# Optimization experiments

Measured on AMD Instinct MI355X. Metric: run time of the kernel, lower is better.

Reference implementation:

```python
import jax, jax.numpy as jnp
import numpy as np

NUM_HEADS = 8
HEAD_DIM = 128
ATTN_SCALE = 0.12


def _rotary_tables(T, head_dim, dtype=jnp.float32):
    # modded-nanogpt half-truncated RoPE: rotate only first half of freq slots
    quarter = head_dim // 4
    angular = (1.0 / 1024.0) ** jnp.linspace(0.0, 1.0, quarter, dtype=dtype)
    angular = jnp.concatenate([angular, jnp.zeros(quarter, dtype=dtype)])  # [head_dim//2]
    t = jnp.arange(T, dtype=dtype)
    theta = t[:, None] * angular[None, :]  # [T, head_dim//2]
    return jnp.cos(theta), jnp.sin(theta)


def _apply_rotary(x, cos, sin):
    # x: [B, T, H, D]; cos/sin: [T, D//2]
    x1, x2 = jnp.split(x, 2, axis=-1)
    c = cos[None, :, None, :]
    s = sin[None, :, None, :]
    y1 = x1 * c + x2 * s
    y2 = -x1 * s + x2 * c
    return jnp.concatenate([y1, y2], axis=-1)


def _rms_norm(x):
    eps = jnp.asarray(jnp.finfo(x.dtype).eps, x.dtype)
    var = jnp.mean(jnp.square(x), axis=-1, keepdims=True)
    return x * jax.lax.rsqrt(var + eps)


def setup_inputs() -> dict:
    key = jax.random.key(0)
    k1, k2, k3, k4, k5 = jax.random.split(key, 5)
    B, T, D = 1, 4096, 1024
    hdim = NUM_HEADS * HEAD_DIM
    std = 0.5 * D ** (-0.5)
    x = jax.random.normal(k1, (B, T, D), dtype=jnp.float32)
    ve = jax.random.normal(k2, (B, T, hdim), dtype=jnp.float32)
    qkv_w = jax.random.normal(k3, (3, hdim, D), dtype=jnp.float32) * std
    lambdas = jnp.array([0.5, 0.5], dtype=jnp.float32)
    c_proj_w = jax.random.normal(k5, (D, hdim), dtype=jnp.float32) * std
    return {"x": x, "ve": ve, "qkv_w": qkv_w, "lambdas": lambdas, "c_proj_w": c_proj_w}


def reference(x, ve, qkv_w, lambdas, c_proj_w):
    B, T, D = x.shape
    H, Hd = NUM_HEADS, HEAD_DIM
    # QKV projection: qkv_w [3, H*Hd, D]
    qkv = jnp.einsum('btd,ckd->btck', x, qkv_w)  # [B, T, 3, H*Hd]
    qkv = qkv.reshape(B, T, 3, H, Hd)
    q, k, v = qkv[:, :, 0], qkv[:, :, 1], qkv[:, :, 2]  # [B, T, H, Hd]
    # QK RMSNorm
    q = _rms_norm(q)
    k = _rms_norm(k)
    # RoPE
    cos, sin = _rotary_tables(T, Hd, dtype=x.dtype)
    q = _apply_rotary(q, cos, sin)
    k = _apply_rotary(k, cos, sin)
    # value-embedding lambda mix
    v = lambdas[0] * v + lambdas[1] * ve.reshape(B, T, H, Hd)
    # causal attention with fixed scale 0.12 (block-causal FlexAttention mask)
    scores = jnp.einsum('bthd,bshd->bhts', q, k) * ATTN_SCALE  # [B, H, T, T]
    causal = jnp.tril(jnp.ones((T, T), dtype=bool))
    scores = jnp.where(causal[None, None], scores, jnp.asarray(-jnp.inf, scores.dtype))
    probs = jax.nn.softmax(scores, axis=-1)
    y = jnp.einsum('bhts,bshd->bthd', probs, v)  # [B, T, H, Hd]
    y = y.reshape(B, T, H * Hd)
    return y @ c_proj_w.T  # [B, T, D]
```

## Files before the change

kernel.cpp:

```cpp
#include <hip/hip_runtime.h>

typedef __bf16 bf16;
typedef __bf16 bf16x8 __attribute__((ext_vector_type(8)));
typedef __bf16 bf16x4 __attribute__((ext_vector_type(4)));
typedef __bf16 bf16x2 __attribute__((ext_vector_type(2)));
typedef float f32x4 __attribute__((ext_vector_type(4)));
typedef float f32x16 __attribute__((ext_vector_type(16)));
typedef int i32x4 __attribute__((ext_vector_type(4)));

#define GLL16(gp, lp)                                                          \
  __builtin_amdgcn_global_load_lds(                                            \
      (const __attribute__((address_space(1))) unsigned int*)(gp),             \
      (__attribute__((address_space(3))) unsigned int*)(lp), 16, 0, 0)

__global__ __launch_bounds__(256) void cast3_f32_bf16(
    const float* __restrict__ a, bf16* __restrict__ oa, int na4,
    const float* __restrict__ b, bf16* __restrict__ ob, int nb4,
    const float* __restrict__ c, bf16* __restrict__ oc, int nc4) {
  int i = blockIdx.x * blockDim.x + threadIdx.x;
  int stride = gridDim.x * blockDim.x;
  int total = na4 + nb4 + nc4;
  for (; i < total; i += stride) {
    const float4* src;
    bf16x4* dst;
    int j = i;
    if (j < na4) {
      src = (const float4*)a + j; dst = (bf16x4*)oa + j;
    } else if ((j -= na4) < nb4) {
      src = (const float4*)b + j; dst = (bf16x4*)ob + j;
    } else {
      j -= nb4;
      src = (const float4*)c + j; dst = (bf16x4*)oc + j;
    }
    float4 v = *src;
    bf16x4 o;
    o[0] = (bf16)v.x; o[1] = (bf16)v.y; o[2] = (bf16)v.z; o[3] = (bf16)v.w;
    *dst = o;
  }
}

template <int K, int LDC, typename CT>
__global__ __launch_bounds__(256) void gemm_bt(
    const bf16* __restrict__ A, const bf16* __restrict__ B,
    CT* __restrict__ C) {
  __shared__ __align__(16) bf16 As[128 * 64];
  __shared__ __align__(16) bf16 Bs[128 * 64];
  const int tid  = threadIdx.x;
  const int lane = tid & 63;
  const int wave = tid >> 6;
  const int ln15 = lane & 15, quad = lane >> 4;
  const int wm = wave >> 1, wn = wave & 1;
  const int m0 = blockIdx.y * 128, n0 = blockIdx.x * 128;

  f32x4 acc[4][4] = {};

  for (int k0 = 0; k0 < K; k0 += 64) {
    __syncthreads();
#pragma unroll
    for (int j = 0; j < 4; ++j) {
      int gbase = j * 256 + wave * 64;
      int g = gbase + lane;
      int r = g >> 3, c = (g & 7) ^ (r & 7);
      GLL16(A + (size_t)(m0 + r) * K + k0 + c * 8, As + (size_t)gbase * 8);
    }
#pragma unroll
    for (int j = 0; j < 4; ++j) {
      int gbase = j * 256 + wave * 64;
      int g = gbase + lane;
      int r = g >> 3, c = (g & 7) ^ (r & 7);
      GLL16(B + (size_t)(n0 + r) * K + k0 + c * 8, Bs + (size_t)gbase * 8);
    }
    __syncthreads();
#pragma unroll
    for (int kk = 0; kk < 2; ++kk) {
      bf16x8 af[4], bfr[4];
#pragma unroll
      for (int mi = 0; mi < 4; ++mi) {
        int m = wm * 64 + mi * 16 + ln15;
        int cg = kk * 4 + quad;
        af[mi] = *(const bf16x8*)(As + (m * 8 + (cg ^ (m & 7))) * 8);
      }
#pragma unroll
      for (int ni = 0; ni < 4; ++ni) {
        int n = wn * 64 + ni * 16 + ln15;
        int cg = kk * 4 + quad;
        bfr[ni] = *(const bf16x8*)(Bs + (n * 8 + (cg ^ (n & 7))) * 8);
      }
#pragma unroll
      for (int mi = 0; mi < 4; ++mi)
#pragma unroll
        for (int ni = 0; ni < 4; ++ni)
          acc[mi][ni] = __builtin_amdgcn_mfma_f32_16x16x32_bf16(
              af[mi], bfr[ni], acc[mi][ni], 0, 0, 0);
    }
  }
#pragma unroll
  for (int mi = 0; mi < 4; ++mi)
#pragma unroll
    for (int ni = 0; ni < 4; ++ni)
#pragma unroll
      for (int r = 0; r < 4; ++r) {
        int row = m0 + wm * 64 + mi * 16 + quad * 4 + r;
        int col = n0 + wn * 64 + ni * 16 + ln15;
        C[(size_t)row * LDC + col] = (CT)acc[mi][ni][r];
      }
}

__global__ __launch_bounds__(256) void qkv_post(
    const bf16* __restrict__ qkv, const float* __restrict__ ve,
    const float* __restrict__ lambdas, bf16* __restrict__ qn,
    bf16* __restrict__ kn, bf16* __restrict__ vt) {
  const int h  = blockIdx.x;
  const int t0 = blockIdx.y * 64;
  const int tid = threadIdx.x;
  const int wave = tid >> 6, lane = tid & 63;
  __shared__ __align__(16) float tile[64][129];

  const int j = lane;
  float cth = 1.0f, sth = 0.0f;
  for (int i = 0; i < 16; ++i) {
    int t = t0 + wave * 16 + i;
    if (j < 32) {
      float ang = exp2f((float)j * (-10.0f / 31.0f));
      float th = (float)t * ang;
      __sincosf(th, &sth, &cth);
    }
#pragma unroll
    for (int qk = 0; qk < 2; ++qk) {
      const bf16* row = qkv + (size_t)t * 3072 + qk * 1024 + h * 128;
      float x1 = (float)row[j], x2 = (float)row[j + 64];
      float ss = x1 * x1 + x2 * x2;
#pragma unroll
      for (int m = 1; m < 64; m <<= 1) ss += __shfl_xor(ss, m, 64);
      float rinv = rsqrtf(ss * (1.0f / 128.0f) + 1.1920929e-7f);
      if (qk == 0) rinv *= 0.12f;
      float y1 = (x1 * cth + x2 * sth) * rinv;
      float y2 = (x2 * cth - x1 * sth) * rinv;
      bf16* orow = (qk == 0 ? qn : kn) + (size_t)t * 1024 + h * 128;
      orow[j] = (bf16)y1;
      orow[j + 64] = (bf16)y2;
    }
  }

  float l0 = lambdas[0], l1 = lambdas[1];
  for (int c = 0; c < 32; ++c) {
    int idx = c * 256 + tid;
    int d = idx & 127, tl = idx >> 7;
    int t = t0 + tl;
    float v = (float)qkv[(size_t)t * 3072 + 2048 + h * 128 + d];
    float vev = ve[(size_t)t * 1024 + h * 128 + d];
    tile[tl][d] = l0 * v + l1 * vev;
  }
  __syncthreads();
  for (int c = 0; c < 32; ++c) {
    int idx = c * 256 + tid;
    int tl = idx & 63, d = idx >> 6;
    vt[((size_t)(h * 128 + d)) * 4096 + t0 + tl] = (bf16)tile[tl][d];
  }
}

__global__ __launch_bounds__(256, 2) void flash_attn(
    const bf16* __restrict__ qn, const bf16* __restrict__ kn,
    const bf16* __restrict__ vt, float* __restrict__ Op,
    float* __restrict__ ls) {
  const int id = blockIdx.x;
  const int qtile = 63 - (id >> 4);
  const int sub = id & 15;
  const int h = sub >> 1;
  const int half = sub & 1;
  const int tid = threadIdx.x;
  const int wave = tid >> 6, lane = tid & 63;
  const int l31 = lane & 31, hl = lane >> 5;
  const int qi = wave >> 1, ki = wave & 1;

  __shared__ __align__(16) bf16 smem[4 * 64 * 128];
  __shared__ float rsb[2][2][32];
  bf16* Ks = smem;
  bf16* Vs = smem + 2 * 64 * 128;

  const int q0 = qtile * 64;
  const int nkv = qtile + 1;
  const int half0 = (nkv + 1) >> 1;
  const int kt_begin = half ? half0 : 0;
  const int kt_end = half ? nkv : half0;
  const int niter = kt_end - kt_begin;
  const int pidx = (h * 64 + qtile) * 2 + half;

  if (niter == 0) {
    float4 z = {0.f, 0.f, 0.f, 0.f};
    float* opb = Op + (size_t)pidx * 8192;
#pragma unroll
    for (int j = 0; j < 8; ++j) *(float4*)(opb + tid * 32 + j * 4) = z;
    if (tid < 64) ls[pidx * 64 + tid] = 0.f;
    return;
  }

  const int qg = q0 + qi * 32 + l31;

  bf16x8 qf[8];
  {
    const bf16* qb = qn + (size_t)qg * 1024 + h * 128 + hl * 8;
#pragma unroll
    for (int f = 0; f < 8; ++f) qf[f] = *(const bf16x8*)(qb + f * 16);
  }

  f32x16 acc_o[4] = {};
  float rs = 0.0f;

  auto prefetch = [&](int kt, int buf) {
    const int kv0 = kt * 64;
    bf16* ks = Ks + buf * (64 * 128);
    bf16* vs = Vs + buf * (128 * 64);
#pragma unroll
    for (int jj = 0; jj < 4; ++jj) {
      int gbase = jj * 256 + wave * 64;
      int g = gbase + lane;
      int r = g >> 4, c = (g & 15) ^ (r & 15);
      GLL16(kn + (size_t)(kv0 + r) * 1024 + h * 128 + c * 8,
            ks + (size_t)gbase * 8);
    }
#pragma unroll
    for (int jj = 0; jj < 4; ++jj) {
      int gbase = jj * 256 + wave * 64;
      int g = gbase + lane;
      int d = g >> 3, c = (g & 7) ^ (d & 7);
      GLL16(vt + ((size_t)(h * 128 + d)) * 4096 + kv0 + c * 8,
            vs + (size_t)gbase * 8);
    }
  };

  prefetch(kt_begin, 0);

  for (int it = 0; it < niter; ++it) {
    const int kt = kt_begin + it;
    const int kv0 = kt * 64;
    __syncthreads();
    if (it + 1 < niter) prefetch(kt + 1, (it + 1) & 1);
    const bf16* ksb = Ks + (it & 1) * (64 * 128);
    const bf16* vsb = Vs + (it & 1) * (128 * 64);

    f32x16 accs = {};
    const int krow = ki * 32 + l31;
#pragma unroll
    for (int f = 0; f < 8; ++f) {
      bf16x8 a =
          *(const bf16x8*)(ksb + (krow * 16 + ((2 * f + hl) ^ (krow & 15))) * 8);
      accs = __builtin_amdgcn_mfma_f32_32x32x16_bf16(a, qf[f], accs, 0, 0, 0);
    }

    const bool diag = (kt == nkv - 1);
    float pe[16];
#pragma unroll
    for (int r = 0; r < 16; ++r) {
      int kvl = (r & 3) + 8 * (r >> 2) + 4 * hl;
      float v = __expf(accs[r]);
      if (diag && (kv0 + ki * 32 + kvl) > qg) v = 0.0f;
      rs += v;
      pe[r] = v;
    }
    int pk[8];
#pragma unroll
    for (int g = 0; g < 8; ++g) {
      bf16x2 t;
      t[0] = (bf16)pe[2 * g];
      t[1] = (bf16)pe[2 * g + 1];
      pk[g] = __builtin_bit_cast(int, t);
    }

    bf16x8 pf[2];
#pragma unroll
    for (int c = 0; c < 2; ++c) {
      int sh0 = __shfl_xor(pk[4 * c + 0], 32, 64);
      int sh1 = __shfl_xor(pk[4 * c + 1], 32, 64);
      int sh2 = __shfl_xor(pk[4 * c + 2], 32, 64);
      int sh3 = __shfl_xor(pk[4 * c + 3], 32, 64);
      int own0 = hl ? pk[4 * c + 2] : pk[4 * c + 0];
      int own1 = hl ? pk[4 * c + 3] : pk[4 * c + 1];
      int par0 = hl ? sh2 : sh0;
      int par1 = hl ? sh3 : sh1;
      i32x4 dv;
      dv[0] = hl ? par0 : own0;
      dv[1] = hl ? par1 : own1;
      dv[2] = hl ? own0 : par0;
      dv[3] = hl ? own1 : par1;
      pf[c] = __builtin_bit_cast(bf16x8, dv);
    }

#pragma unroll
    for (int dt = 0; dt < 4; ++dt) {
      int vrow = dt * 32 + l31;
#pragma unroll
      for (int c = 0; c < 2; ++c) {
        bf16x8 a = *(const bf16x8*)(
            vsb + (vrow * 8 + ((4 * ki + 2 * c + hl) ^ (vrow & 7))) * 8);
        acc_o[dt] =
            __builtin_amdgcn_mfma_f32_32x32x16_bf16(a, pf[c], acc_o[dt], 0, 0, 0);
      }
    }
  }

  rs += __shfl_xor(rs, 32, 64);
  __syncthreads();
  if (lane < 32) rsb[qi][ki][l31] = rs;
  float* ob = (float*)smem;
  if (ki == 1) {
#pragma unroll
    for (int dt = 0; dt < 4; ++dt)
#pragma unroll
      for (int r = 0; r < 16; ++r) {
        int d = dt * 32 + (r & 3) + 8 * (r >> 2) + 4 * hl;
        ob[(qi * 32 + l31) * 129 + d] = acc_o[dt][r];
      }
  }
  __syncthreads();
  if (ki == 0) {
    float lsum = rsb[qi][0][l31] + rsb[qi][1][l31];
    if (hl == 0) ls[pidx * 64 + qi * 32 + l31] = lsum;
    float* opb = Op + (size_t)pidx * 8192 + (qi * 32 + l31) * 128;
#pragma unroll
    for (int dt = 0; dt < 4; ++dt)
#pragma unroll
      for (int rg = 0; rg < 4; ++rg) {
        float4 o;
        int d0 = dt * 32 + 4 * hl + 8 * rg;
        o.x = acc_o[dt][rg * 4 + 0] + ob[(qi * 32 + l31) * 129 + d0 + 0];
        o.y = acc_o[dt][rg * 4 + 1] + ob[(qi * 32 + l31) * 129 + d0 + 1];
        o.z = acc_o[dt][rg * 4 + 2] + ob[(qi * 32 + l31) * 129 + d0 + 2];
        o.w = acc_o[dt][rg * 4 + 3] + ob[(qi * 32 + l31) * 129 + d0 + 3];
        *(float4*)(opb + d0) = o;
      }
  }
}

__global__ __launch_bounds__(256) void attn_combine(
    const float* __restrict__ Op, const float* __restrict__ ls,
    bf16* __restrict__ y) {
  int gid = blockIdx.x * 256 + threadIdx.x;
  int t = gid >> 8;
  int c4 = gid & 255;
  int qtile = t >> 6, ql = t & 63;
  int h = c4 >> 5;
  int d = (c4 & 31) * 4;
  int pbase = (h * 64 + qtile) * 2;
  const float4 o0 = *(const float4*)(Op + (size_t)pbase * 8192 + ql * 128 + d);
  const float4 o1 =
      *(const float4*)(Op + (size_t)(pbase + 1) * 8192 + ql * 128 + d);
  float inv = 1.0f / (ls[pbase * 64 + ql] + ls[(pbase + 1) * 64 + ql]);
  bf16x4 o;
  o[0] = (bf16)((o0.x + o1.x) * inv);
  o[1] = (bf16)((o0.y + o1.y) * inv);
  o[2] = (bf16)((o0.z + o1.z) * inv);
  o[3] = (bf16)((o0.w + o1.w) * inv);
  *(bf16x4*)(y + (size_t)t * 1024 + h * 128 + d) = o;
}

extern "C" void kernel_launch(void* const* d_in, const int* in_sizes, int n_in,
                              void* d_out, int out_size, void* d_ws,
                              size_t ws_size, hipStream_t stream) {
  const float* x       = (const float*)d_in[0];
  const float* ve      = (const float*)d_in[1];
  const float* qkv_w   = (const float*)d_in[2];
  const float* lambdas = (const float*)d_in[3];
  const float* c_proj  = (const float*)d_in[4];
  float* out = (float*)d_out;

  char* ws = (char*)d_ws;
  bf16* qkv   = (bf16*)ws;
  bf16* xbf   = (bf16*)(ws + 25165824);
  bf16* wqkv  = (bf16*)(ws + 33554432);
  bf16* wproj = (bf16*)(ws + 39845888);
  bf16* qn    = (bf16*)(ws + 41943040);
  bf16* kn    = (bf16*)(ws + 50331648);
  bf16* vt    = (bf16*)(ws + 58720256);
  bf16* yb    = (bf16*)(ws + 67108864);
  float* Op  = (float*)ws;
  float* lsw = (float*)(ws + 33554432);

  cast3_f32_bf16<<<2048, 256, 0, stream>>>(x, xbf, 4194304 / 4, qkv_w, wqkv,
                                           3145728 / 4, c_proj, wproj,
                                           1048576 / 4);

  gemm_bt<1024, 3072, bf16><<<dim3(24, 32), 256, 0, stream>>>(xbf, wqkv, qkv);

  qkv_post<<<dim3(8, 64), 256, 0, stream>>>(qkv, ve, lambdas, qn, kn, vt);

  flash_attn<<<1024, 256, 0, stream>>>(qn, kn, vt, Op, lsw);
  attn_combine<<<4096, 256, 0, stream>>>(Op, lsw, yb);

  gemm_bt<1024, 1024, float><<<dim3(8, 32), 256, 0, stream>>>(yb, wproj, out);
}
```

Measured before the change: 239.9 us.

## Single-buffer V through registers to cut LDS and raise attention occupancy

V tiles are no longer double-buffered in LDS via direct global-to-LDS loads. They are loaded into registers during the current iteration and written to a single LDS buffer after an extra barrier, with a new swizzle. This shrinks shared memory from 64KB to 48KB so launch bounds can request 3 blocks per CU instead of 2. The P-fragment exchange also switches to permlane32_swap when that builtin exists, replacing shuffles and selects. The cost is extra VGPR pressure from holding V in registers plus a second barrier per iteration, under a tighter register budget from the higher occupancy target.

```diff
diff --git a/kernel.cpp b/kernel.cpp
--- a/kernel.cpp
+++ b/kernel.cpp
@@ -7,6 +7,7 @@
 typedef float f32x4 __attribute__((ext_vector_type(4)));
 typedef float f32x16 __attribute__((ext_vector_type(16)));
 typedef int i32x4 __attribute__((ext_vector_type(4)));
+typedef int i32x2 __attribute__((ext_vector_type(2)));
 
 #define GLL16(gp, lp)                                                          \
   __builtin_amdgcn_global_load_lds(                                            \
@@ -159,7 +160,7 @@
   }
 }
 
-__global__ __launch_bounds__(256, 2) void flash_attn(
+__global__ __launch_bounds__(256, 3) void flash_attn(
     const bf16* __restrict__ qn, const bf16* __restrict__ kn,
     const bf16* __restrict__ vt, float* __restrict__ Op,
     float* __restrict__ ls) {
@@ -173,7 +174,7 @@
   const int l31 = lane & 31, hl = lane >> 5;
   const int qi = wave >> 1, ki = wave & 1;
 
-  __shared__ __align__(16) bf16 smem[4 * 64 * 128];
+  __shared__ __align__(16) bf16 smem[3 * 64 * 128];
   __shared__ float rsb[2][2][32];
   bf16* Ks = smem;
   bf16* Vs = smem + 2 * 64 * 128;
@@ -206,11 +207,11 @@
 
   f32x16 acc_o[4] = {};
   float rs = 0.0f;
-
-  auto prefetch = [&](int kt, int buf) {
+  bf16x8 vreg[4];
+
+  auto prefetch_k = [&](int kt, int buf) {
     const int kv0 = kt * 64;
     bf16* ks = Ks + buf * (64 * 128);
-    bf16* vs = Vs + buf * (128 * 64);
 #pragma unroll
     for (int jj = 0; jj < 4; ++jj) {
       int gbase = jj * 256 + wave * 64;
@@ -219,25 +220,41 @@
       GLL16(kn + (size_t)(kv0 + r) * 1024 + h * 128 + c * 8,
             ks + (size_t)gbase * 8);
     }
+  };
+  auto load_v = [&](int kt) {
+    const int kv0 = kt * 64;
 #pragma unroll
     for (int jj = 0; jj < 4; ++jj) {
-      int gbase = jj * 256 + wave * 64;
-      int g = gbase + lane;
-      int d = g >> 3, c = (g & 7) ^ (d & 7);
-      GLL16(vt + ((size_t)(h * 128 + d)) * 4096 + kv0 + c * 8,
-            vs + (size_t)gbase * 8);
+      int g = jj * 256 + tid;
+      int d = g >> 3, c = g & 7;
+      vreg[jj] =
+          *(const bf16x8*)(vt + ((size_t)(h * 128 + d)) * 4096 + kv0 + c * 8);
     }
   };
-
-  prefetch(kt_begin, 0);
+  auto store_v = [&]() {
+#pragma unroll
+    for (int jj = 0; jj < 4; ++jj) {
+      int g = jj * 256 + tid;
+      int d = g >> 3, c = g & 7;
+      int pos = (((d & 1) << 3) | c) ^ (d & 7);
+      *(bf16x8*)(Vs + (d >> 1) * 128 + pos * 8) = vreg[jj];
+    }
+  };
+
+  prefetch_k(kt_begin, 0);
+  load_v(kt_begin);
+  store_v();
 
   for (int it = 0; it < niter; ++it) {
     const int kt = kt_begin + it;
     const int kv0 = kt * 64;
     __syncthreads();
-    if (it + 1 < niter) prefetch(kt + 1, (it + 1) & 1);
+    const bool more = (it + 1 < niter);
+    if (more) {
+      prefetch_k(kt + 1, (it + 1) & 1);
+      load_v(kt + 1);
+    }
     const bf16* ksb = Ks + (it & 1) * (64 * 128);
-    const bf16* vsb = Vs + (it & 1) * (128 * 64);
 
     f32x16 accs = {};
     const int krow = ki * 32 + l31;
@@ -268,6 +285,21 @@
     }
 
     bf16x8 pf[2];
+#if __has_builtin(__builtin_amdgcn_permlane32_swap)
+#pragma unroll
+    for (int c = 0; c < 2; ++c) {
+      i32x2 r02 = __builtin_amdgcn_permlane32_swap(pk[4 * c + 0], pk[4 * c + 2],
+                                                   false, false);
+      i32x2 r13 = __builtin_amdgcn_permlane32_swap(pk[4 * c + 1], pk[4 * c + 3],
+                                                   false, false);
+      i32x4 dv;
+      dv[0] = r02[0];
+      dv[1] = r13[0];
+      dv[2] = r02[1];
+      dv[3] = r13[1];
+      pf[c] = __builtin_bit_cast(bf16x8, dv);
+    }
+#else
 #pragma unroll
     for (int c = 0; c < 2; ++c) {
       int sh0 = __shfl_xor(pk[4 * c + 0], 32, 64);
@@ -285,17 +317,24 @@
       dv[3] = hl ? own1 : par1;
       pf[c] = __builtin_bit_cast(bf16x8, dv);
     }
+#endif
 
 #pragma unroll
     for (int dt = 0; dt < 4; ++dt) {
       int vrow = dt * 32 + l31;
 #pragma unroll
       for (int c = 0; c < 2; ++c) {
-        bf16x8 a = *(const bf16x8*)(
-            vsb + (vrow * 8 + ((4 * ki + 2 * c + hl) ^ (vrow & 7))) * 8);
+        int g8 = 4 * ki + 2 * c + hl;
+        int pos = (((vrow & 1) << 3) | g8) ^ (vrow & 7);
+        bf16x8 a = *(const bf16x8*)(Vs + (vrow >> 1) * 128 + pos * 8);
         acc_o[dt] =
             __builtin_amdgcn_mfma_f32_32x32x16_bf16(a, pf[c], acc_o[dt], 0, 0, 0);
       }
+    }
+
+    if (more) {
+      __syncthreads();
+      store_v();
     }
   }
 
```

Result: slower. 275.1 us (+14.7%).
